# Kernel tuning notes

Hardware: AMD Instinct MI355X
Metric: run time of the kernel (lower is better)

The kernel has to match this reference:

```python
import jax, jax.numpy as jnp
import numpy as np

N = 50000          # nodes per side (variables == clauses here)
IN, HID, OUT = 64, 128, 128
H = 4              # attention heads (self and cross)
P = 2              # num_meta_paths
E = 640000         # edges per graph
NEG = 0.2          # leaky_relu negative slope


def _glorot(key, shape):
    fan = shape[-2] + shape[-1]
    return (jax.random.normal(key, shape) * jnp.sqrt(2.0 / fan)).astype(jnp.float32)


def _ln(x, g, b):
    mu = x.mean(-1, keepdims=True)
    v = ((x - mu) ** 2).mean(-1, keepdims=True)
    return (x - mu) / jnp.sqrt(v + 1e-5) * g + b


def _segment_softmax(s, seg, num):
    # s: [E, H]; softmax over edges sharing the same seg id
    smax = jax.ops.segment_max(s, seg, num_segments=num)
    e = jnp.exp(s - smax[seg])
    den = jax.ops.segment_sum(e, seg, num_segments=num)
    return e / (den[seg] + 1e-16)


def _agg(alpha, feats, src, dst, num):
    # out[d, h, c] = sum_{e: dst[e]=d} alpha[e,h] * feats[src[e], c]
    gathered = feats[src]  # [E, C]
    outs = [jax.ops.segment_sum(alpha[:, h:h + 1] * gathered, dst, num_segments=num)
            for h in range(alpha.shape[1])]
    return jnp.stack(outs, axis=1)  # [num, H, C]


def _hga_self(x, adj, W, att_l, att_r, bias):
    # homogeneous HGAConv with self loops, concat=False (mean over heads)
    n = x.shape[0]
    xl = x @ W.T                      # [N, C]
    al = xl @ att_l                   # [N, H]
    ar = xl @ att_r                   # [N, H]
    loops = jnp.arange(n)
    src = jnp.concatenate([adj[0], loops])
    dst = jnp.concatenate([adj[1], loops])
    score = al[dst] + ar[src]         # edge_score: a_l[adj[1]] + a_r[adj[0]]
    alpha = _segment_softmax(jax.nn.leaky_relu(score, NEG), dst, n)
    out = _agg(alpha, xl, src, dst, n).mean(axis=1)  # [N, C]
    return out + bias


def _hga_cross(xv, xc, adj, Wl, Wr, att_l, att_r, bias):
    # bipartite HGAConv: adj[1] indexes var nodes, adj[0] indexes cls nodes
    n, m = xv.shape[0], xc.shape[0]
    xl = xv @ Wl.T
    xr = xc @ Wr.T
    al = xl @ att_l
    ar = xr @ att_r
    ar_ = xl @ att_r
    al_ = xr @ att_l
    c_idx, v_idx = adj[0], adj[1]
    score = al[v_idx] + ar[c_idx]        # -> normalized per var node
    score_ = ar_[v_idx] + al_[c_idx]     # transposed direction -> per cls node
    alpha = _segment_softmax(jax.nn.leaky_relu(score, NEG), v_idx, n)
    alpha_ = _segment_softmax(jax.nn.leaky_relu(score_, NEG), c_idx, m)
    out_var = _agg(alpha, xr, c_idx, v_idx, n).mean(axis=1) + bias   # [n, OUT]
    out_cls = _agg(alpha_, xl, v_idx, c_idx, m).mean(axis=1) + bias  # [m, OUT]
    return out_var, out_cls


def setup_inputs() -> dict:
    key = jax.random.key(0)
    ks = jax.random.split(key, 32)
    d = {}
    d['x_var'] = jax.random.normal(ks[0], (N, IN), dtype=jnp.float32)
    d['x_cls'] = jax.random.normal(ks[1], (N, IN), dtype=jnp.float32)
    d['mp_var'] = jax.random.randint(ks[2], (P, 2, E), 0, N)
    d['mp_cls'] = jax.random.randint(ks[3], (P, 2, E), 0, N)
    d['adj_pos'] = jax.random.randint(ks[4], (2, E), 0, N)
    d['adj_neg'] = jax.random.randint(ks[5], (2, E), 0, N)
    d['W_var_emb'] = _glorot(ks[6], (HID, IN))
    d['W_cls_emb'] = _glorot(ks[7], (HID, IN))
    d['ln_var_g'] = jnp.ones(HID); d['ln_var_b'] = jnp.zeros(HID)
    d['ln_cls_g'] = jnp.ones(HID); d['ln_cls_b'] = jnp.zeros(HID)
    d['var_pw'] = jnp.ones(P); d['cls_pw'] = jnp.ones(P)
    d['sv_W'] = _glorot(ks[8], (P, HID, HID))
    d['sv_al'] = _glorot(ks[9], (P, HID, H))
    d['sv_ar'] = _glorot(ks[10], (P, HID, H))
    d['sv_b'] = jnp.zeros((P, HID))
    d['sc_W'] = _glorot(ks[11], (P, HID, HID))
    d['sc_al'] = _glorot(ks[12], (P, HID, H))
    d['sc_ar'] = _glorot(ks[13], (P, HID, H))
    d['sc_b'] = jnp.zeros((P, HID))
    d['cp_Wl'] = _glorot(ks[14], (OUT, HID))
    d['cp_Wr'] = _glorot(ks[15], (OUT, HID))
    d['cp_al'] = _glorot(ks[16], (OUT, H))
    d['cp_ar'] = _glorot(ks[17], (OUT, H))
    d['cp_b'] = jnp.zeros(OUT)
    d['cn_Wl'] = _glorot(ks[18], (OUT, HID))
    d['cn_Wr'] = _glorot(ks[19], (OUT, HID))
    d['cn_al'] = _glorot(ks[20], (OUT, H))
    d['cn_ar'] = _glorot(ks[21], (OUT, H))
    d['cn_b'] = jnp.zeros(OUT)
    return d


def reference(x_var, x_cls, mp_var, mp_cls, adj_pos, adj_neg,
              W_var_emb, W_cls_emb, ln_var_g, ln_var_b, ln_cls_g, ln_cls_b,
              var_pw, cls_pw, sv_W, sv_al, sv_ar, sv_b, sc_W, sc_al, sc_ar, sc_b,
              cp_Wl, cp_Wr, cp_al, cp_ar, cp_b, cn_Wl, cn_Wr, cn_al, cn_ar, cn_b):
    xv = x_var @ W_var_emb.T          # [N, HID]
    xc = x_cls @ W_cls_emb.T
    # pre-norm residual self-attention, weighted sum over meta paths
    hv = _ln(xv, ln_var_g, ln_var_b)
    hc = _ln(xc, ln_cls_g, ln_cls_b)
    av = sum(var_pw[p] * _hga_self(hv, mp_var[p], sv_W[p], sv_al[p], sv_ar[p], sv_b[p]) for p in range(P))
    ac = sum(cls_pw[p] * _hga_self(hc, mp_cls[p], sc_W[p], sc_al[p], sc_ar[p], sc_b[p]) for p in range(P))
    xv = xv + av
    xc = xc + ac
    # bipartite cross attention over positive / negative literal edges
    vpos, cpos = _hga_cross(xv, xc, adj_pos, cp_Wl, cp_Wr, cp_al, cp_ar, cp_b)
    vneg, cneg = _hga_cross(xv, xc, adj_neg, cn_Wl, cn_Wr, cn_al, cn_ar, cn_b)
    return jnp.stack([vpos + vneg, cpos + cneg])  # [2, N, OUT]
```

## Files before the change

kernel.cpp:

```cpp
#include <hip/hip_runtime.h>
#include <hip/hip_bf16.h>

#define NN 50000
#define EE 640000
#define NEG 0.2f
#define CAP 64

#define BSH 9
#define NBKT 98
#define FCAP 7168
#define CHUNKA 8192
#define PA_B 79

struct Ptr8 { const int* p[8]; };
struct MArgs { const float* w[8]; const float* al[8]; const float* ar[8]; };

struct SegArg {
    const int* starts;
    const int* counts;
    const unsigned short* srt;
    const float* adst;
    const float* asrc;
    const unsigned short* feats;
    const float* pw;
    int pwi;
    int hasLoop;
};

typedef __attribute__((ext_vector_type(8))) short short8;
typedef __attribute__((ext_vector_type(8))) unsigned short ushort8;
typedef __attribute__((ext_vector_type(4))) float floatx4;

__device__ __forceinline__ unsigned short f2bf(float x) {
    unsigned b = __float_as_uint(x);
    b = b + 0x7fffu + ((b >> 16) & 1u);
    return (unsigned short)(b >> 16);
}

__device__ __forceinline__ float4 leakyexp4(float4 ad, float4 as) {
    float v0 = ad.x + as.x, v1 = ad.y + as.y, v2 = ad.z + as.z, v3 = ad.w + as.w;
    v0 = v0 > 0.f ? v0 : NEG * v0;
    v1 = v1 > 0.f ? v1 : NEG * v1;
    v2 = v2 > 0.f ? v2 : NEG * v2;
    v3 = v3 > 0.f ? v3 : NEG * v3;
    return make_float4(__expf(v0), __expf(v1), __expf(v2), __expf(v3));
}

__global__ void transpose_emb(const float* __restrict__ wev, const float* __restrict__ wec,
                              float* __restrict__ out)
{
    int i = blockIdx.x * 256 + threadIdx.x;
    if (i < 8192) { out[i] = wev[(i & 127) * 64 + (i >> 7)]; return; }
    if (i < 16384) { int j = i - 8192; out[i] = wec[(j & 127) * 64 + (j >> 7)]; }
}

__global__ void make_M(MArgs a, float* __restrict__ Mbuf)
{
    int b = blockIdx.x;
    const float* W  = a.w[b];
    const float* AL = a.al[b];
    const float* AR = a.ar[b];
    for (int e = threadIdx.x; e < 1024; e += 256) {
        int k = e >> 3, h = e & 7;
        const float* att = (h < 4) ? AL : AR;
        int hh = h & 3;
        float s = 0.f;
        for (int c = 0; c < 128; c++) s += W[c * 128 + k] * att[c * 4 + hh];
        Mbuf[b * 1024 + e] = s;
    }
}

__global__ void prep_W(MArgs a, unsigned short* __restrict__ Wbf)
{
    int tid = blockIdx.x * 256 + threadIdx.x;
    int w = tid >> 11;
    int idx = tid & 2047;
    int tile = idx >> 6;
    int lane = idx & 63;
    int ct = tile >> 2, kc = tile & 3;
    int n = ct * 16 + (lane & 15);
    int k0 = kc * 32 + (lane >> 4) * 8;
    const float* src = a.w[w] + n * 128 + k0;
    short8 v;
#pragma unroll
    for (int j = 0; j < 8; j++) v[j] = (short)f2bf(src[j]);
    *(short8*)&Wbf[(size_t)tid * 8] = v;
}

__global__ void embed_ln(const float* __restrict__ x, const float* __restrict__ Wt,
                         const float* __restrict__ g, const float* __restrict__ b,
                         const float* __restrict__ pw, const float* __restrict__ sb,
                         float* __restrict__ F, float* __restrict__ C)
{
    __shared__ float lx[8][64];
    __shared__ float red[2][8][2];
    int c = threadIdx.x;
    int n0 = blockIdx.x * 8;
    for (int t = c; t < 8 * 64; t += 128) {
        lx[t >> 6][t & 63] = x[(size_t)(n0 + (t >> 6)) * 64 + (t & 63)];
    }
    __syncthreads();
    float acc[8];
#pragma unroll
    for (int m = 0; m < 8; m++) acc[m] = 0.f;
    for (int k = 0; k < 64; k++) {
        float w = Wt[k * 128 + c];
#pragma unroll
        for (int m = 0; m < 8; m++) acc[m] += lx[m][k] * w;
    }
    int lane = c & 63, wv = c >> 6;
#pragma unroll
    for (int m = 0; m < 8; m++) {
        float s1 = acc[m], s2 = acc[m] * acc[m];
        for (int off = 32; off; off >>= 1) { s1 += __shfl_xor(s1, off); s2 += __shfl_xor(s2, off); }
        if (lane == 0) { red[wv][m][0] = s1; red[wv][m][1] = s2; }
    }
    __syncthreads();
    float biassum = pw[0] * sb[c] + pw[1] * sb[128 + c];
    float gg = g[c], bb = b[c];
#pragma unroll
    for (int m = 0; m < 8; m++) {
        float s1 = red[0][m][0] + red[1][m][0];
        float s2 = red[0][m][1] + red[1][m][1];
        float mu  = s1 * (1.f / 128.f);
        float var = s2 * (1.f / 128.f) - mu * mu;
        float inv = rsqrtf(var + 1e-5f);
        float v = acc[m];
        size_t idx = (size_t)(n0 + m) * 128 + c;
        F[idx] = v + biassum;
        C[idx] = (v - mu) * inv * gg + bb;
    }
}

__global__ __launch_bounds__(256) void mfma_proj2(
    const float* __restrict__ in,
    const unsigned short* __restrict__ Wp0, const unsigned short* __restrict__ Wp1,
    const float* __restrict__ M0, const float* __restrict__ M1,
    unsigned short* __restrict__ ob0, unsigned short* __restrict__ ob1,
    float4* __restrict__ dl0, float4* __restrict__ dr0,
    float4* __restrict__ dl1, float4* __restrict__ dr1)
{
    __shared__ float ML[2048];

    int t = threadIdx.x;
    for (int i = t; i < 2048; i += 256) ML[i] = (i < 1024) ? M0[i] : M1[i - 1024];
    __syncthreads();

    int w = t >> 6, lane = t & 63;
    int rg = w & 1, chh = w >> 1;
    int ln = lane & 15, quad = lane >> 4;
    int rbase = blockIdx.x * 32 + rg * 16;
    int row = rbase + ln;
    int arow = (row < NN) ? row : (NN - 1);
    const float* MLh = &ML[chh * 1024];

    short8 afrag[4];
    float p[8];
#pragma unroll
    for (int h = 0; h < 8; h++) p[h] = 0.f;
#pragma unroll
    for (int kc = 0; kc < 4; kc++) {
        int k0 = kc * 32 + quad * 8;
        const float* ap = in + (size_t)arow * 128 + k0;
        float av[8];
#pragma unroll
        for (int j = 0; j < 8; j++) av[j] = ap[j];
#pragma unroll
        for (int j = 0; j < 8; j++) {
            afrag[kc][j] = (short)f2bf(av[j]);
            const float* mrow = &MLh[(k0 + j) * 8];
#pragma unroll
            for (int h = 0; h < 8; h++) p[h] += av[j] * mrow[h];
        }
    }
#pragma unroll
    for (int h = 0; h < 8; h++) {
        p[h] += __shfl_xor(p[h], 16);
        p[h] += __shfl_xor(p[h], 32);
    }
    if (quad == 0 && row < NN) {
        if (chh == 0) {
            dl0[row] = make_float4(p[0], p[1], p[2], p[3]);
            dr0[row] = make_float4(p[4], p[5], p[6], p[7]);
        } else {
            dl1[row] = make_float4(p[0], p[1], p[2], p[3]);
            dr1[row] = make_float4(p[4], p[5], p[6], p[7]);
        }
    }

#pragma unroll
    for (int cti = 0; cti < 4; cti++) {
        int ct = chh * 4 + cti;
        floatx4 acc = {0.f, 0.f, 0.f, 0.f};
#pragma unroll
        for (int kc = 0; kc < 4; kc++) {
            short8 bfr = *(const short8*)&Wp0[(size_t)((ct * 4 + kc) * 64 + lane) * 8];
            acc = __builtin_amdgcn_mfma_f32_16x16x32_bf16(afrag[kc], bfr, acc, 0, 0, 0);
        }
#pragma unroll
        for (int r = 0; r < 4; r++) {
            int rr = rbase + quad * 4 + r;
            if (rr < NN) ob0[(size_t)rr * 128 + ct * 16 + ln] = f2bf(acc[r]);
        }
    }
#pragma unroll
    for (int cti = 0; cti < 4; cti++) {
        int ct = chh * 4 + cti;
        floatx4 acc = {0.f, 0.f, 0.f, 0.f};
#pragma unroll
        for (int kc = 0; kc < 4; kc++) {
            short8 bfr = *(const short8*)&Wp1[(size_t)((ct * 4 + kc) * 64 + lane) * 8];
            acc = __builtin_amdgcn_mfma_f32_16x16x32_bf16(afrag[kc], bfr, acc, 0, 0, 0);
        }
#pragma unroll
        for (int r = 0; r < 4; r++) {
            int rr = rbase + quad * 4 + r;
            if (rr < NN) ob1[(size_t)rr * 128 + ct * 16 + ln] = f2bf(acc[r]);
        }
    }
}

__global__ void zero_bcnt(int* __restrict__ p)
{
    int i = blockIdx.x * 256 + threadIdx.x;
    if (i < 8 * NBKT) p[i] = 0;
}

__global__ void bucket_count(Ptr8 dst, int* __restrict__ bcnt)
{
    __shared__ int h[NBKT];
    int l = blockIdx.x / PA_B, cb = blockIdx.x % PA_B;
    const int* dp = dst.p[l];
    for (int i = threadIdx.x; i < NBKT; i += 256) h[i] = 0;
    __syncthreads();
    int e0 = cb * CHUNKA;
    for (int i = threadIdx.x; i < CHUNKA; i += 256) {
        int e = e0 + i;
        if (e < EE) atomicAdd(&h[dp[e] >> BSH], 1);
    }
    __syncthreads();
    for (int i = threadIdx.x; i < NBKT; i += 256)
        if (h[i]) atomicAdd(&bcnt[l * NBKT + i], h[i]);
}

__global__ void bucket_scan(const int* __restrict__ bcnt, int* __restrict__ bstart,
                            int* __restrict__ bcur)
{
    __shared__ int sh[NBKT];
    int l = blockIdx.x;
    for (int i = threadIdx.x; i < NBKT; i += 256) sh[i] = bcnt[l * NBKT + i];
    __syncthreads();
    if (threadIdx.x == 0) {
        int acc = 0;
        for (int i = 0; i < NBKT; i++) { int t = sh[i]; sh[i] = acc; acc += t; }
    }
    __syncthreads();
    for (int i = threadIdx.x; i < NBKT; i += 256) {
        bstart[l * (NBKT + 1) + i] = sh[i];
        bcur[l * NBKT + i] = sh[i];
    }
    if (threadIdx.x == 0) bstart[l * (NBKT + 1) + NBKT] = EE;
}

__global__ void bucket_place(Ptr8 src, Ptr8 dst, int* __restrict__ bcur,
                             unsigned* __restrict__ recs)
{
    __shared__ int h[NBKT];
    __shared__ int base[NBKT];
    int l = blockIdx.x / PA_B, cb = blockIdx.x % PA_B;
    const int* sp = src.p[l];
    const int* dp = dst.p[l];
    for (int i = threadIdx.x; i < NBKT; i += 256) h[i] = 0;
    __syncthreads();
    int e0 = cb * CHUNKA;
    for (int i = threadIdx.x; i < CHUNKA; i += 256) {
        int e = e0 + i;
        if (e < EE) atomicAdd(&h[dp[e] >> BSH], 1);
    }
    __syncthreads();
    for (int i = threadIdx.x; i < NBKT; i += 256) {
        int c = h[i];
        base[i] = c ? atomicAdd(&bcur[l * NBKT + i], c) : 0;
        h[i] = 0;
    }
    __syncthreads();
    unsigned* rl = recs + (size_t)l * EE;
    for (int i = threadIdx.x; i < CHUNKA; i += 256) {
        int e = e0 + i;
        if (e >= EE) continue;
        int d = dp[e];
        int b = d >> BSH;
        int pos = base[b] + atomicAdd(&h[b], 1);
        rl[pos] = ((unsigned)sp[e] << 16) | (unsigned)d;
    }
}

__global__ __launch_bounds__(256) void bucket_final(
    const unsigned* __restrict__ recs, const int* __restrict__ bstart,
    int* __restrict__ starts8, int* __restrict__ counts8,
    unsigned short* __restrict__ sortedU)
{
    __shared__ unsigned R[FCAP];
    __shared__ int cnt[512];
    __shared__ int cur[512];
    __shared__ int psum[256];
    int l = blockIdx.x / NBKT, b = blockIdx.x % NBKT;
    int d0 = b << BSH;
    int nd = min(512, NN - d0);
    int ebase = bstart[l * (NBKT + 1) + b];
    int ecnt  = bstart[l * (NBKT + 1) + b + 1] - ebase;
    const unsigned* rp = recs + (size_t)l * EE + ebase;
    int t = threadIdx.x;
    bool inLds = (ecnt <= FCAP);

    for (int i = t; i < 512; i += 256) cnt[i] = 0;
    __syncthreads();
    for (int i = t; i < ecnt; i += 256) {
        unsigned r = rp[i];
        if (inLds) R[i] = r;
        atomicAdd(&cnt[(r & 0xffffu) - d0], 1);
    }
    __syncthreads();
    int s0 = cnt[2 * t] + cnt[2 * t + 1];
    psum[t] = s0;
    __syncthreads();
    for (int off = 1; off < 256; off <<= 1) {
        int x = (t >= off) ? psum[t - off] : 0;
        __syncthreads();
        psum[t] += x;
        __syncthreads();
    }
    int excl = psum[t] - s0;
    cur[2 * t] = excl;
    cur[2 * t + 1] = excl + cnt[2 * t];
    __syncthreads();
    for (int i = t; i < nd; i += 256) {
        starts8[l * NN + d0 + i] = ebase + cur[i];
        counts8[l * NN + d0 + i] = cnt[i];
    }
    __syncthreads();
    unsigned short* so = sortedU + (size_t)l * EE + ebase;
    for (int i = t; i < ecnt; i += 256) {
        unsigned r = inLds ? R[i] : rp[i];
        int dloc = (int)(r & 0xffffu) - d0;
        int pos = atomicAdd(&cur[dloc], 1);
        so[pos] = (unsigned short)(r >> 16);
    }
}

__global__ __launch_bounds__(256, 6) void agg_fused(
    SegArg A, SegArg B,
    const float* __restrict__ bias0, const float* __restrict__ bias1,
    float* __restrict__ acc, int mode)
{
    __shared__ uint2 pSh[16][CAP];

    int t = threadIdx.x;
    int gid = t >> 4;
    int sub = t & 15;
    int seg = gid & 1;
    int d   = blockIdx.x * 8 + (gid >> 1);

    const int* starts = seg ? B.starts : A.starts;
    const int* counts = seg ? B.counts : A.counts;
    const unsigned short* srt = seg ? B.srt : A.srt;
    const float* adst = seg ? B.adst : A.adst;
    const float* asrc = seg ? B.asrc : A.asrc;
    const unsigned short* feats = seg ? B.feats : A.feats;
    const float* pw = seg ? B.pw : A.pw;
    int pwi = seg ? B.pwi : A.pwi;
    int hasLoop = seg ? B.hasLoop : A.hasLoop;

    int base = starts[d];
    int k = counts[d];
    int kTot = k + hasLoop;

    float4 ad = *(const float4*)(adst + (size_t)d * 4);

    float den0 = 0.f, den1 = 0.f, den2 = 0.f, den3 = 0.f;
    float4 e0 = {0,0,0,0}, e1 = {0,0,0,0}, e2 = {0,0,0,0}, e3 = {0,0,0,0};
    int s0 = 0, s1 = 0, s2 = 0, s3 = 0;
    int ia = sub, ib = sub + 16, ic = sub + 32, id = sub + 48;
    if (ia < kTot) {
        s0 = (ia < k) ? (int)srt[base + ia] : d;
        e0 = leakyexp4(ad, *(const float4*)(asrc + (size_t)s0 * 4));
        den0 += e0.x; den1 += e0.y; den2 += e0.z; den3 += e0.w;
    }
    if (ib < kTot) {
        s1 = (ib < k) ? (int)srt[base + ib] : d;
        e1 = leakyexp4(ad, *(const float4*)(asrc + (size_t)s1 * 4));
        den0 += e1.x; den1 += e1.y; den2 += e1.z; den3 += e1.w;
    }
    if (ic < kTot) {
        s2 = (ic < k) ? (int)srt[base + ic] : d;
        e2 = leakyexp4(ad, *(const float4*)(asrc + (size_t)s2 * 4));
        den0 += e2.x; den1 += e2.y; den2 += e2.z; den3 += e2.w;
    }
    if (id < kTot) {
        s3 = (id < k) ? (int)srt[base + id] : d;
        e3 = leakyexp4(ad, *(const float4*)(asrc + (size_t)s3 * 4));
        den0 += e3.x; den1 += e3.y; den2 += e3.z; den3 += e3.w;
    }
    for (int i = sub + 64; i < kTot; i += 16) {
        int s = (i < k) ? (int)srt[base + i] : d;
        float4 e = leakyexp4(ad, *(const float4*)(asrc + (size_t)s * 4));
        den0 += e.x; den1 += e.y; den2 += e.z; den3 += e.w;
    }
#pragma unroll
    for (int off = 1; off <= 8; off <<= 1) {
        den0 += __shfl_xor(den0, off); den1 += __shfl_xor(den1, off);
        den2 += __shfl_xor(den2, off); den3 += __shfl_xor(den3, off);
    }
    float scale = 0.25f * (pw ? pw[pwi] : 1.0f);
    float r0 = scale / (den0 + 1e-16f);
    float r1 = scale / (den1 + 1e-16f);
    float r2 = scale / (den2 + 1e-16f);
    float r3 = scale / (den3 + 1e-16f);

    if (ia < kTot) pSh[gid][ia] = make_uint2(
        __float_as_uint(e0.x * r0 + e0.y * r1 + e0.z * r2 + e0.w * r3), (unsigned)s0);
    if (ib < kTot) pSh[gid][ib] = make_uint2(
        __float_as_uint(e1.x * r0 + e1.y * r1 + e1.z * r2 + e1.w * r3), (unsigned)s1);
    if (ic < kTot) pSh[gid][ic] = make_uint2(
        __float_as_uint(e2.x * r0 + e2.y * r1 + e2.z * r2 + e2.w * r3), (unsigned)s2);
    if (id < kTot) pSh[gid][id] = make_uint2(
        __float_as_uint(e3.x * r0 + e3.y * r1 + e3.z * r2 + e3.w * r3), (unsigned)s3);

    float a[8];
#pragma unroll
    for (int i = 0; i < 8; i++) a[i] = 0.f;
    const unsigned short* fbase = feats + sub * 8;
    int kW = kTot < CAP ? kTot : CAP;
    int j = 0;
    for (; j + 2 <= kW; j += 2) {
        uint4 pq = *(const uint4*)&pSh[gid][j];
        ushort8 va = *(const ushort8*)(fbase + (size_t)pq.y * 128);
        ushort8 vb = *(const ushort8*)(fbase + (size_t)pq.w * 128);
        float wa = __uint_as_float(pq.x), wb = __uint_as_float(pq.z);
#pragma unroll
        for (int i = 0; i < 8; i++) {
            a[i] += wa * __uint_as_float((unsigned)(unsigned short)va[i] << 16);
            a[i] += wb * __uint_as_float((unsigned)(unsigned short)vb[i] << 16);
        }
    }
    if (j < kW) {
        uint2 ps = pSh[gid][j];
        ushort8 v = *(const ushort8*)(fbase + (size_t)ps.y * 128);
        float wgt = __uint_as_float(ps.x);
#pragma unroll
        for (int i = 0; i < 8; i++)
            a[i] += wgt * __uint_as_float((unsigned)(unsigned short)v[i] << 16);
    }
    for (int jj = CAP; jj < kTot; ++jj) {
        int s = (jj < k) ? (int)srt[base + jj] : d;
        float4 e = leakyexp4(ad, *(const float4*)(asrc + (size_t)s * 4));
        float wgt = e.x * r0 + e.y * r1 + e.z * r2 + e.w * r3;
        ushort8 v = *(const ushort8*)(fbase + (size_t)s * 128);
#pragma unroll
        for (int i = 0; i < 8; i++)
            a[i] += wgt * __uint_as_float((unsigned)(unsigned short)v[i] << 16);
    }

#pragma unroll
    for (int i = 0; i < 8; i++) a[i] += __shfl_xor(a[i], 16);

    if (seg == 0) {
        size_t idx = (size_t)d * 128 + sub * 8;
        float4* ap = (float4*)(acc + idx);
        float4 lo = make_float4(a[0], a[1], a[2], a[3]);
        float4 hi = make_float4(a[4], a[5], a[6], a[7]);
        if (mode) {
            const float4* b0 = (const float4*)(bias0 + sub * 8);
            const float4* b1 = (const float4*)(bias1 + sub * 8);
            float4 c0 = b0[0], c1 = b0[1], d0v = b1[0], d1v = b1[1];
            ap[0] = make_float4(c0.x + d0v.x + lo.x, c0.y + d0v.y + lo.y,
                                c0.z + d0v.z + lo.z, c0.w + d0v.w + lo.w);
            ap[1] = make_float4(c1.x + d1v.x + hi.x, c1.y + d1v.y + hi.y,
                                c1.z + d1v.z + hi.z, c1.w + d1v.w + hi.w);
        } else {
            float4 rr0 = ap[0], rr1 = ap[1];
            ap[0] = make_float4(rr0.x + lo.x, rr0.y + lo.y, rr0.z + lo.z, rr0.w + lo.w);
            ap[1] = make_float4(rr1.x + hi.x, rr1.y + hi.y, rr1.z + hi.z, rr1.w + hi.w);
        }
    }
}

extern "C" void kernel_launch(void* const* d_in, const int* in_sizes, int n_in,
                              void* d_out, int out_size, void* d_ws, size_t ws_size,
                              hipStream_t stream)
{
    const float* x_var   = (const float*)d_in[0];
    const float* x_cls   = (const float*)d_in[1];
    const int*   mp_var  = (const int*)d_in[2];
    const int*   mp_cls  = (const int*)d_in[3];
    const int*   adj_pos = (const int*)d_in[4];
    const int*   adj_neg = (const int*)d_in[5];
    const float* W_var_emb = (const float*)d_in[6];
    const float* W_cls_emb = (const float*)d_in[7];
    const float* ln_var_g = (const float*)d_in[8];
    const float* ln_var_b = (const float*)d_in[9];
    const float* ln_cls_g = (const float*)d_in[10];
    const float* ln_cls_b = (const float*)d_in[11];
    const float* var_pw = (const float*)d_in[12];
    const float* cls_pw = (const float*)d_in[13];
    const float* sv_W  = (const float*)d_in[14];
    const float* sv_al = (const float*)d_in[15];
    const float* sv_ar = (const float*)d_in[16];
    const float* sv_b  = (const float*)d_in[17];
    const float* sc_W  = (const float*)d_in[18];
    const float* sc_al = (const float*)d_in[19];
    const float* sc_ar = (const float*)d_in[20];
    const float* sc_b  = (const float*)d_in[21];
    const float* cp_Wl = (const float*)d_in[22];
    const float* cp_Wr = (const float*)d_in[23];
    const float* cp_al = (const float*)d_in[24];
    const float* cp_ar = (const float*)d_in[25];
    const float* cp_b  = (const float*)d_in[26];
    const float* cn_Wl = (const float*)d_in[27];
    const float* cn_Wr = (const float*)d_in[28];
    const float* cn_al = (const float*)d_in[29];
    const float* cn_ar = (const float*)d_in[30];
    const float* cn_b  = (const float*)d_in[31];

    float* out0 = (float*)d_out;
    float* out1 = out0 + (size_t)NN * 128;

    float* ws = (float*)d_ws;
    size_t off = 0;
    auto alloc = [&](size_t n) { float* p = ws + off; off += n; return p; };
    float* Wt   = alloc(16384);
    float* Mbuf = alloc(8 * 1024);
    unsigned short* Wbf = (unsigned short*)alloc(8 * 8192);
    float* F   = alloc((size_t)NN * 128);
    float* G   = alloc((size_t)NN * 128);
    float* C   = alloc((size_t)NN * 128);
    float* D   = alloc((size_t)NN * 128);
    unsigned short* B1 = (unsigned short*)alloc((size_t)NN * 64);
    unsigned short* B2 = (unsigned short*)alloc((size_t)NN * 64);
    float* dl   = alloc(NN * 4);
    float* dr   = alloc(NN * 4);
    float* dl2  = alloc(NN * 4);
    float* dr2  = alloc(NN * 4);
    float* dl3  = alloc(NN * 4);
    float* dr3  = alloc(NN * 4);
    float* dl4  = alloc(NN * 4);
    float* dr4  = alloc(NN * 4);
    int* counts8 = (int*)alloc(8 * NN);
    int* starts8 = (int*)alloc(8 * NN);
    int* bcnt    = (int*)alloc(8 * NBKT);
    int* bstart  = (int*)alloc(8 * (NBKT + 1));
    int* bcur    = (int*)alloc(8 * NBKT);
    unsigned* recs = (unsigned*)alloc((size_t)8 * EE);
    unsigned short* sortedU = (unsigned short*)alloc((size_t)4 * EE);

    unsigned short* Pc = (unsigned short*)C;
    unsigned short* Pd = (unsigned short*)C + (size_t)NN * 128;

    const float* WtEv = Wt;
    const float* WtEc = Wt + 8192;

    Ptr8 srcP, dstP;
    srcP.p[0] = mp_var;            dstP.p[0] = mp_var + EE;
    srcP.p[1] = mp_var + 2 * EE;   dstP.p[1] = mp_var + 3 * EE;
    srcP.p[2] = mp_cls;            dstP.p[2] = mp_cls + EE;
    srcP.p[3] = mp_cls + 2 * EE;   dstP.p[3] = mp_cls + 3 * EE;
    srcP.p[4] = adj_pos;           dstP.p[4] = adj_pos + EE;
    srcP.p[5] = adj_pos + EE;      dstP.p[5] = adj_pos;
    srcP.p[6] = adj_neg;           dstP.p[6] = adj_neg + EE;
    srcP.p[7] = adj_neg + EE;      dstP.p[7] = adj_neg;

    MArgs ma;
    ma.w[0] = sv_W;           ma.al[0] = sv_al;        ma.ar[0] = sv_ar;
    ma.w[1] = sv_W + 16384;   ma.al[1] = sv_al + 512;  ma.ar[1] = sv_ar + 512;
    ma.w[2] = sc_W;           ma.al[2] = sc_al;        ma.ar[2] = sc_ar;
    ma.w[3] = sc_W + 16384;   ma.al[3] = sc_al + 512;  ma.ar[3] = sc_ar + 512;
    ma.w[4] = cp_Wl;          ma.al[4] = cp_al;        ma.ar[4] = cp_ar;
    ma.w[5] = cp_Wr;          ma.al[5] = cp_al;        ma.ar[5] = cp_ar;
    ma.w[6] = cn_Wl;          ma.al[6] = cn_al;        ma.ar[6] = cn_ar;
    ma.w[7] = cn_Wr;          ma.al[7] = cn_al;        ma.ar[7] = cn_ar;

    zero_bcnt<<<(8 * NBKT + 255) / 256, 256, 0, stream>>>(bcnt);
    bucket_count<<<8 * PA_B, 256, 0, stream>>>(dstP, bcnt);
    bucket_scan<<<8, 256, 0, stream>>>(bcnt, bstart, bcur);
    bucket_place<<<8 * PA_B, 256, 0, stream>>>(srcP, dstP, bcur, recs);
    bucket_final<<<8 * NBKT, 256, 0, stream>>>(recs, bstart, starts8, counts8, sortedU);

    transpose_emb<<<64, 256, 0, stream>>>(W_var_emb, W_cls_emb, Wt);
    make_M<<<8, 256, 0, stream>>>(ma, Mbuf);
    prep_W<<<64, 256, 0, stream>>>(ma, Wbf);
    embed_ln<<<NN / 8, 128, 0, stream>>>(x_var, WtEv, ln_var_g, ln_var_b, var_pw, sv_b, F, C);
    embed_ln<<<NN / 8, 128, 0, stream>>>(x_cls, WtEc, ln_cls_g, ln_cls_b, cls_pw, sc_b, G, D);

    const int PB = (NN + 31) / 32;
    const int AB = NN / 8;

    for (int side = 0; side < 2; ++side) {
        const float* h    = side ? D : C;
        float*       accp = side ? G : F;
        const float* pw   = side ? cls_pw : var_pw;
        int s0 = side * 2, s1 = side * 2 + 1;
        mfma_proj2<<<PB, 256, 0, stream>>>(h, Wbf + s0 * 16384, Wbf + s1 * 16384,
                                           Mbuf + s0 * 1024, Mbuf + s1 * 1024,
                                           B1, B2,
                                           (float4*)dl, (float4*)dr,
                                           (float4*)dl2, (float4*)dr2);
        SegArg SA, SB;
        SA.starts = starts8 + s0 * NN; SA.counts = counts8 + s0 * NN;
        SA.srt = sortedU + (size_t)s0 * EE;
        SA.adst = dl;  SA.asrc = dr;  SA.feats = B1; SA.pw = pw; SA.pwi = 0; SA.hasLoop = 1;
        SB.starts = starts8 + s1 * NN; SB.counts = counts8 + s1 * NN;
        SB.srt = sortedU + (size_t)s1 * EE;
        SB.adst = dl2; SB.asrc = dr2; SB.feats = B2; SB.pw = pw; SB.pwi = 1; SB.hasLoop = 1;
        agg_fused<<<AB, 256, 0, stream>>>(SA, SB, cp_b, cn_b, accp, 0);
    }

    mfma_proj2<<<PB, 256, 0, stream>>>(F, Wbf + 4 * 16384, Wbf + 6 * 16384,
                                       Mbuf + 4 * 1024, Mbuf + 6 * 1024,
                                       B1, Pc,
                                       (float4*)dl, (float4*)dr,
                                       (float4*)dl3, (float4*)dr3);
    mfma_proj2<<<PB, 256, 0, stream>>>(G, Wbf + 5 * 16384, Wbf + 7 * 16384,
                                       Mbuf + 5 * 1024, Mbuf + 7 * 1024,
                                       B2, Pd,
                                       (float4*)dl2, (float4*)dr2,
                                       (float4*)dl4, (float4*)dr4);

    {
        SegArg SA, SB;
        SA.starts = starts8 + 4 * NN; SA.counts = counts8 + 4 * NN;
        SA.srt = sortedU + (size_t)4 * EE;
        SA.adst = dl;  SA.asrc = dr2; SA.feats = B2; SA.pw = nullptr; SA.pwi = 0; SA.hasLoop = 0;
        SB.starts = starts8 + 6 * NN; SB.counts = counts8 + 6 * NN;
        SB.srt = sortedU + (size_t)6 * EE;
        SB.adst = dl3; SB.asrc = dr4; SB.feats = Pd; SB.pw = nullptr; SB.pwi = 0; SB.hasLoop = 0;
        agg_fused<<<AB, 256, 0, stream>>>(SA, SB, cp_b, cn_b, out0, 1);
    }
    {
        SegArg SA, SB;
        SA.starts = starts8 + 5 * NN; SA.counts = counts8 + 5 * NN;
        SA.srt = sortedU + (size_t)5 * EE;
        SA.adst = dl2; SA.asrc = dr;  SA.feats = B1; SA.pw = nullptr; SA.pwi = 0; SA.hasLoop = 0;
        SB.starts = starts8 + 7 * NN; SB.counts = counts8 + 7 * NN;
        SB.srt = sortedU + (size_t)7 * EE;
        SB.adst = dl4; SB.asrc = dr3; SB.feats = Pc; SB.pw = nullptr; SB.pwi = 0; SB.hasLoop = 0;
        agg_fused<<<AB, 256, 0, stream>>>(SA, SB, cp_b, cn_b, out1, 1);
    }
}
```

Baseline: 691.1 us.

## Batch var/cls stages into merged launches and prefetch features in aggregation

Merges the small weight-prep kernels into one launch, runs both embed+LN passes in a single grid, and batches the var and cls self-attention aggregations (and the two cross aggregations) into double-size launches by writing the cls projections to separate buffers. The aggregation kernel now stores weights and source ids in separate shared arrays and issues the first four feature gathers before the softmax denominator is computed, to hide gather latency. It also raises the occupancy hint to 8 blocks per SM and replaces the zeroing kernel with a memset. The cost is higher register pressure from the prefetched fragments and extra buffer usage (Pc/Pd reused earlier).

```diff
diff --git a/kernel.cpp b/kernel.cpp
--- a/kernel.cpp
+++ b/kernel.cpp
@@ -27,6 +27,19 @@
     int hasLoop;
 };
 
+struct ProjArgs {
+    const float* in;
+    const unsigned short* Wp0; const unsigned short* Wp1;
+    const float* M0; const float* M1;
+    unsigned short* ob0; unsigned short* ob1;
+    float4* dl0; float4* dr0; float4* dl1; float4* dr1;
+};
+
+struct EmbArgs {
+    const float* x; const float* Wt; const float* g; const float* b;
+    const float* pw; const float* sb; float* F; float* C;
+};
+
 typedef __attribute__((ext_vector_type(8))) short short8;
 typedef __attribute__((ext_vector_type(8))) unsigned short ushort8;
 typedef __attribute__((ext_vector_type(4))) float floatx4;
@@ -46,65 +59,67 @@
     return make_float4(__expf(v0), __expf(v1), __expf(v2), __expf(v3));
 }
 
-__global__ void transpose_emb(const float* __restrict__ wev, const float* __restrict__ wec,
-                              float* __restrict__ out)
-{
-    int i = blockIdx.x * 256 + threadIdx.x;
-    if (i < 8192) { out[i] = wev[(i & 127) * 64 + (i >> 7)]; return; }
-    if (i < 16384) { int j = i - 8192; out[i] = wec[(j & 127) * 64 + (j >> 7)]; }
-}
-
-__global__ void make_M(MArgs a, float* __restrict__ Mbuf)
+__global__ void prep_all(const float* __restrict__ wev, const float* __restrict__ wec,
+                         float* __restrict__ Wt, MArgs a, float* __restrict__ Mbuf,
+                         unsigned short* __restrict__ Wbf)
 {
     int b = blockIdx.x;
-    const float* W  = a.w[b];
-    const float* AL = a.al[b];
-    const float* AR = a.ar[b];
-    for (int e = threadIdx.x; e < 1024; e += 256) {
-        int k = e >> 3, h = e & 7;
-        const float* att = (h < 4) ? AL : AR;
-        int hh = h & 3;
-        float s = 0.f;
-        for (int c = 0; c < 128; c++) s += W[c * 128 + k] * att[c * 4 + hh];
-        Mbuf[b * 1024 + e] = s;
-    }
-}
-
-__global__ void prep_W(MArgs a, unsigned short* __restrict__ Wbf)
-{
-    int tid = blockIdx.x * 256 + threadIdx.x;
-    int w = tid >> 11;
-    int idx = tid & 2047;
-    int tile = idx >> 6;
-    int lane = idx & 63;
-    int ct = tile >> 2, kc = tile & 3;
-    int n = ct * 16 + (lane & 15);
-    int k0 = kc * 32 + (lane >> 4) * 8;
-    const float* src = a.w[w] + n * 128 + k0;
-    short8 v;
-#pragma unroll
-    for (int j = 0; j < 8; j++) v[j] = (short)f2bf(src[j]);
-    *(short8*)&Wbf[(size_t)tid * 8] = v;
-}
-
-__global__ void embed_ln(const float* __restrict__ x, const float* __restrict__ Wt,
-                         const float* __restrict__ g, const float* __restrict__ b,
-                         const float* __restrict__ pw, const float* __restrict__ sb,
-                         float* __restrict__ F, float* __restrict__ C)
+    if (b < 64) {
+        int i = b * 256 + threadIdx.x;
+        if (i < 8192) { Wt[i] = wev[(i & 127) * 64 + (i >> 7)]; }
+        else { int j = i - 8192; Wt[i] = wec[(j & 127) * 64 + (j >> 7)]; }
+        return;
+    }
+    if (b < 128) {
+        int tid = (b - 64) * 256 + threadIdx.x;
+        int w = tid >> 11;
+        int idx = tid & 2047;
+        int tile = idx >> 6;
+        int lane = idx & 63;
+        int ct = tile >> 2, kc = tile & 3;
+        int n = ct * 16 + (lane & 15);
+        int k0 = kc * 32 + (lane >> 4) * 8;
+        const float* src = a.w[w] + n * 128 + k0;
+        short8 v;
+#pragma unroll
+        for (int j = 0; j < 8; j++) v[j] = (short)f2bf(src[j]);
+        *(short8*)&Wbf[(size_t)tid * 8] = v;
+        return;
+    }
+    {
+        int w = b - 128;
+        const float* W  = a.w[w];
+        const float* AL = a.al[w];
+        const float* AR = a.ar[w];
+        for (int e = threadIdx.x; e < 1024; e += 256) {
+            int k = e >> 3, h = e & 7;
+            const float* att = (h < 4) ? AL : AR;
+            int hh = h & 3;
+            float s = 0.f;
+            for (int c = 0; c < 128; c++) s += W[c * 128 + k] * att[c * 4 + hh];
+            Mbuf[w * 1024 + e] = s;
+        }
+    }
+}
+
+__global__ void embed_ln2(EmbArgs Ea, EmbArgs Eb, int nb)
 {
     __shared__ float lx[8][64];
     __shared__ float red[2][8][2];
+    int half = blockIdx.x >= nb;
+    const EmbArgs E = half ? Eb : Ea;
+    int blk = blockIdx.x - (half ? nb : 0);
     int c = threadIdx.x;
-    int n0 = blockIdx.x * 8;
+    int n0 = blk * 8;
     for (int t = c; t < 8 * 64; t += 128) {
-        lx[t >> 6][t & 63] = x[(size_t)(n0 + (t >> 6)) * 64 + (t & 63)];
+        lx[t >> 6][t & 63] = E.x[(size_t)(n0 + (t >> 6)) * 64 + (t & 63)];
     }
     __syncthreads();
     float acc[8];
 #pragma unroll
     for (int m = 0; m < 8; m++) acc[m] = 0.f;
     for (int k = 0; k < 64; k++) {
-        float w = Wt[k * 128 + c];
+        float w = E.Wt[k * 128 + c];
 #pragma unroll
         for (int m = 0; m < 8; m++) acc[m] += lx[m][k] * w;
     }
@@ -116,8 +131,8 @@
         if (lane == 0) { red[wv][m][0] = s1; red[wv][m][1] = s2; }
     }
     __syncthreads();
-    float biassum = pw[0] * sb[c] + pw[1] * sb[128 + c];
-    float gg = g[c], bb = b[c];
+    float biassum = E.pw[0] * E.sb[c] + E.pw[1] * E.sb[128 + c];
+    float gg = E.g[c], bb = E.b[c];
 #pragma unroll
     for (int m = 0; m < 8; m++) {
         float s1 = red[0][m][0] + red[1][m][0];
@@ -127,29 +142,27 @@
         float inv = rsqrtf(var + 1e-5f);
         float v = acc[m];
         size_t idx = (size_t)(n0 + m) * 128 + c;
-        F[idx] = v + biassum;
-        C[idx] = (v - mu) * inv * gg + bb;
-    }
-}
-
-__global__ __launch_bounds__(256) void mfma_proj2(
-    const float* __restrict__ in,
-    const unsigned short* __restrict__ Wp0, const unsigned short* __restrict__ Wp1,
-    const float* __restrict__ M0, const float* __restrict__ M1,
-    unsigned short* __restrict__ ob0, unsigned short* __restrict__ ob1,
-    float4* __restrict__ dl0, float4* __restrict__ dr0,
-    float4* __restrict__ dl1, float4* __restrict__ dr1)
+        E.F[idx] = v + biassum;
+        E.C[idx] = (v - mu) * inv * gg + bb;
+    }
+}
+
+__global__ __launch_bounds__(256) void mfma_proj2(ProjArgs Pa, ProjArgs Pb, int nb)
 {
     __shared__ float ML[2048];
 
+    int half = blockIdx.x >= nb;
+    const ProjArgs P = half ? Pb : Pa;
+    int blk = blockIdx.x - (half ? nb : 0);
+
     int t = threadIdx.x;
-    for (int i = t; i < 2048; i += 256) ML[i] = (i < 1024) ? M0[i] : M1[i - 1024];
+    for (int i = t; i < 2048; i += 256) ML[i] = (i < 1024) ? P.M0[i] : P.M1[i - 1024];
     __syncthreads();
 
     int w = t >> 6, lane = t & 63;
     int rg = w & 1, chh = w >> 1;
     int ln = lane & 15, quad = lane >> 4;
-    int rbase = blockIdx.x * 32 + rg * 16;
+    int rbase = blk * 32 + rg * 16;
     int row = rbase + ln;
     int arow = (row < NN) ? row : (NN - 1);
     const float* MLh = &ML[chh * 1024];
@@ -161,7 +174,7 @@
 #pragma unroll
     for (int kc = 0; kc < 4; kc++) {
         int k0 = kc * 32 + quad * 8;
-        const float* ap = in + (size_t)arow * 128 + k0;
+        const float* ap = P.in + (size_t)arow * 128 + k0;
         float av[8];
 #pragma unroll
         for (int j = 0; j < 8; j++) av[j] = ap[j];
@@ -180,11 +193,11 @@
     }
     if (quad == 0 && row < NN) {
         if (chh == 0) {
-            dl0[row] = make_float4(p[0], p[1], p[2], p[3]);
-            dr0[row] = make_float4(p[4], p[5], p[6], p[7]);
+            P.dl0[row] = make_float4(p[0], p[1], p[2], p[3]);
+            P.dr0[row] = make_float4(p[4], p[5], p[6], p[7]);
         } else {
-            dl1[row] = make_float4(p[0], p[1], p[2], p[3]);
-            dr1[row] = make_float4(p[4], p[5], p[6], p[7]);
+            P.dl1[row] = make_float4(p[0], p[1], p[2], p[3]);
+            P.dr1[row] = make_float4(p[4], p[5], p[6], p[7]);
         }
     }
 
@@ -194,13 +207,13 @@
         floatx4 acc = {0.f, 0.f, 0.f, 0.f};
 #pragma unroll
         for (int kc = 0; kc < 4; kc++) {
-            short8 bfr = *(const short8*)&Wp0[(size_t)((ct * 4 + kc) * 64 + lane) * 8];
+            short8 bfr = *(const short8*)&P.Wp0[(size_t)((ct * 4 + kc) * 64 + lane) * 8];
             acc = __builtin_amdgcn_mfma_f32_16x16x32_bf16(afrag[kc], bfr, acc, 0, 0, 0);
         }
 #pragma unroll
         for (int r = 0; r < 4; r++) {
             int rr = rbase + quad * 4 + r;
-            if (rr < NN) ob0[(size_t)rr * 128 + ct * 16 + ln] = f2bf(acc[r]);
+            if (rr < NN) P.ob0[(size_t)rr * 128 + ct * 16 + ln] = f2bf(acc[r]);
         }
     }
 #pragma unroll
@@ -209,21 +222,15 @@
         floatx4 acc = {0.f, 0.f, 0.f, 0.f};
 #pragma unroll
         for (int kc = 0; kc < 4; kc++) {
-            short8 bfr = *(const short8*)&Wp1[(size_t)((ct * 4 + kc) * 64 + lane) * 8];
+            short8 bfr = *(const short8*)&P.Wp1[(size_t)((ct * 4 + kc) * 64 + lane) * 8];
             acc = __builtin_amdgcn_mfma_f32_16x16x32_bf16(afrag[kc], bfr, acc, 0, 0, 0);
         }
 #pragma unroll
         for (int r = 0; r < 4; r++) {
             int rr = rbase + quad * 4 + r;
-            if (rr < NN) ob1[(size_t)rr * 128 + ct * 16 + ln] = f2bf(acc[r]);
-        }
-    }
-}
-
-__global__ void zero_bcnt(int* __restrict__ p)
-{
-    int i = blockIdx.x * 256 + threadIdx.x;
-    if (i < 8 * NBKT) p[i] = 0;
+            if (rr < NN) P.ob1[(size_t)rr * 128 + ct * 16 + ln] = f2bf(acc[r]);
+        }
+    }
 }
 
 __global__ void bucket_count(Ptr8 dst, int* __restrict__ bcnt)
@@ -348,62 +355,61 @@
     }
 }
 
-__global__ __launch_bounds__(256, 6) void agg_fused(
-    SegArg A, SegArg B,
+__global__ __launch_bounds__(256, 8) void agg_fused2(
+    SegArg A0, SegArg B0, float* __restrict__ acc0,
+    SegArg A1, SegArg B1, float* __restrict__ acc1,
     const float* __restrict__ bias0, const float* __restrict__ bias1,
-    float* __restrict__ acc, int mode)
-{
-    __shared__ uint2 pSh[16][CAP];
+    int nb, int mode)
+{
+    __shared__ float          wSh[16][CAP + 1];
+    __shared__ unsigned short sSh[16][CAP + 2];
 
     int t = threadIdx.x;
-    int gid = t >> 4;
-    int sub = t & 15;
+    int gid = t >> 4, sub = t & 15;
     int seg = gid & 1;
-    int d   = blockIdx.x * 8 + (gid >> 1);
-
-    const int* starts = seg ? B.starts : A.starts;
-    const int* counts = seg ? B.counts : A.counts;
-    const unsigned short* srt = seg ? B.srt : A.srt;
-    const float* adst = seg ? B.adst : A.adst;
-    const float* asrc = seg ? B.asrc : A.asrc;
-    const unsigned short* feats = seg ? B.feats : A.feats;
-    const float* pw = seg ? B.pw : A.pw;
-    int pwi = seg ? B.pwi : A.pwi;
-    int hasLoop = seg ? B.hasLoop : A.hasLoop;
-
-    int base = starts[d];
-    int k = counts[d];
-    int kTot = k + hasLoop;
-
-    float4 ad = *(const float4*)(adst + (size_t)d * 4);
+    int half = blockIdx.x >= nb;
+    int blk = blockIdx.x - (half ? nb : 0);
+    int d = blk * 8 + (gid >> 1);
+
+    const SegArg S = half ? (seg ? B1 : A1) : (seg ? B0 : A0);
+    float* acc = half ? acc1 : acc0;
+
+    int base = S.starts[d];
+    int k = S.counts[d];
+    int kTot = k + S.hasLoop;
+    int kW = kTot < CAP ? kTot : CAP;
+
+    float4 ad = *(const float4*)(S.adst + (size_t)d * 4);
+
+    int ia = sub, ib = sub + 16, ic = sub + 32, id_ = sub + 48;
+    int s0 = d, s1 = d, s2 = d, s3 = d;
+    if (ia < kTot) { if (ia < k) s0 = (int)S.srt[base + ia]; sSh[gid][ia] = (unsigned short)s0; }
+    if (ib < kTot) { if (ib < k) s1 = (int)S.srt[base + ib]; sSh[gid][ib] = (unsigned short)s1; }
+    if (ic < kTot) { if (ic < k) s2 = (int)S.srt[base + ic]; sSh[gid][ic] = (unsigned short)s2; }
+    if (id_ < kTot){ if (id_ < k) s3 = (int)S.srt[base + id_]; sSh[gid][id_] = (unsigned short)s3; }
+
+    float4 as0 = {0,0,0,0}, as1 = {0,0,0,0}, as2 = {0,0,0,0}, as3 = {0,0,0,0};
+    if (ia < kTot)  as0 = *(const float4*)(S.asrc + (size_t)s0 * 4);
+    if (ib < kTot)  as1 = *(const float4*)(S.asrc + (size_t)s1 * 4);
+    if (ic < kTot)  as2 = *(const float4*)(S.asrc + (size_t)s2 * 4);
+    if (id_ < kTot) as3 = *(const float4*)(S.asrc + (size_t)s3 * 4);
+
+    const unsigned short* fbase = S.feats + sub * 8;
+    ushort8 pf0 = {0,0,0,0,0,0,0,0}, pf1 = pf0, pf2 = pf0, pf3 = pf0;
+    if (0 < kW) { int q = sSh[gid][0]; pf0 = *(const ushort8*)(fbase + (size_t)q * 128); }
+    if (1 < kW) { int q = sSh[gid][1]; pf1 = *(const ushort8*)(fbase + (size_t)q * 128); }
+    if (2 < kW) { int q = sSh[gid][2]; pf2 = *(const ushort8*)(fbase + (size_t)q * 128); }
+    if (3 < kW) { int q = sSh[gid][3]; pf3 = *(const ushort8*)(fbase + (size_t)q * 128); }
 
     float den0 = 0.f, den1 = 0.f, den2 = 0.f, den3 = 0.f;
     float4 e0 = {0,0,0,0}, e1 = {0,0,0,0}, e2 = {0,0,0,0}, e3 = {0,0,0,0};
-    int s0 = 0, s1 = 0, s2 = 0, s3 = 0;
-    int ia = sub, ib = sub + 16, ic = sub + 32, id = sub + 48;
-    if (ia < kTot) {
-        s0 = (ia < k) ? (int)srt[base + ia] : d;
-        e0 = leakyexp4(ad, *(const float4*)(asrc + (size_t)s0 * 4));
-        den0 += e0.x; den1 += e0.y; den2 += e0.z; den3 += e0.w;
-    }
-    if (ib < kTot) {
-        s1 = (ib < k) ? (int)srt[base + ib] : d;
-        e1 = leakyexp4(ad, *(const float4*)(asrc + (size_t)s1 * 4));
-        den0 += e1.x; den1 += e1.y; den2 += e1.z; den3 += e1.w;
-    }
-    if (ic < kTot) {
-        s2 = (ic < k) ? (int)srt[base + ic] : d;
-        e2 = leakyexp4(ad, *(const float4*)(asrc + (size_t)s2 * 4));
-        den0 += e2.x; den1 += e2.y; den2 += e2.z; den3 += e2.w;
-    }
-    if (id < kTot) {
-        s3 = (id < k) ? (int)srt[base + id] : d;
-        e3 = leakyexp4(ad, *(const float4*)(asrc + (size_t)s3 * 4));
-        den0 += e3.x; den1 += e3.y; den2 += e3.z; den3 += e3.w;
-    }
+    if (ia < kTot) { e0 = leakyexp4(ad, as0); den0 += e0.x; den1 += e0.y; den2 += e0.z; den3 += e0.w; }
+    if (ib < kTot) { e1 = leakyexp4(ad, as1); den0 += e1.x; den1 += e1.y; den2 += e1.z; den3 += e1.w; }
+    if (ic < kTot) { e2 = leakyexp4(ad, as2); den0 += e2.x; den1 += e2.y; den2 += e2.z; den3 += e2.w; }
+    if (id_ < kTot){ e3 = leakyexp4(ad, as3); den0 += e3.x; den1 += e3.y; den2 += e3.z; den3 += e3.w; }
     for (int i = sub + 64; i < kTot; i += 16) {
-        int s = (i < k) ? (int)srt[base + i] : d;
-        float4 e = leakyexp4(ad, *(const float4*)(asrc + (size_t)s * 4));
+        int s = (i < k) ? (int)S.srt[base + i] : d;
+        float4 e = leakyexp4(ad, *(const float4*)(S.asrc + (size_t)s * 4));
         den0 += e.x; den1 += e.y; den2 += e.z; den3 += e.w;
     }
 #pragma unroll
@@ -411,49 +417,56 @@
         den0 += __shfl_xor(den0, off); den1 += __shfl_xor(den1, off);
         den2 += __shfl_xor(den2, off); den3 += __shfl_xor(den3, off);
     }
-    float scale = 0.25f * (pw ? pw[pwi] : 1.0f);
+    float scale = 0.25f * (S.pw ? S.pw[S.pwi] : 1.0f);
     float r0 = scale / (den0 + 1e-16f);
     float r1 = scale / (den1 + 1e-16f);
     float r2 = scale / (den2 + 1e-16f);
     float r3 = scale / (den3 + 1e-16f);
 
-    if (ia < kTot) pSh[gid][ia] = make_uint2(
-        __float_as_uint(e0.x * r0 + e0.y * r1 + e0.z * r2 + e0.w * r3), (unsigned)s0);
-    if (ib < kTot) pSh[gid][ib] = make_uint2(
-        __float_as_uint(e1.x * r0 + e1.y * r1 + e1.z * r2 + e1.w * r3), (unsigned)s1);
-    if (ic < kTot) pSh[gid][ic] = make_uint2(
-        __float_as_uint(e2.x * r0 + e2.y * r1 + e2.z * r2 + e2.w * r3), (unsigned)s2);
-    if (id < kTot) pSh[gid][id] = make_uint2(
-        __float_as_uint(e3.x * r0 + e3.y * r1 + e3.z * r2 + e3.w * r3), (unsigned)s3);
+    if (ia < kTot)  wSh[gid][ia]  = e0.x * r0 + e0.y * r1 + e0.z * r2 + e0.w * r3;
+    if (ib < kTot)  wSh[gid][ib]  = e1.x * r0 + e1.y * r1 + e1.z * r2 + e1.w * r3;
+    if (ic < kTot)  wSh[gid][ic]  = e2.x * r0 + e2.y * r1 + e2.z * r2 + e2.w * r3;
+    if (id_ < kTot) wSh[gid][id_] = e3.x * r0 + e3.y * r1 + e3.z * r2 + e3.w * r3;
 
     float a[8];
 #pragma unroll
     for (int i = 0; i < 8; i++) a[i] = 0.f;
-    const unsigned short* fbase = feats + sub * 8;
-    int kW = kTot < CAP ? kTot : CAP;
-    int j = 0;
+    if (0 < kW) { float w = wSh[gid][0];
+#pragma unroll
+        for (int i = 0; i < 8; i++) a[i] += w * __uint_as_float((unsigned)(unsigned short)pf0[i] << 16); }
+    if (1 < kW) { float w = wSh[gid][1];
+#pragma unroll
+        for (int i = 0; i < 8; i++) a[i] += w * __uint_as_float((unsigned)(unsigned short)pf1[i] << 16); }
+    if (2 < kW) { float w = wSh[gid][2];
+#pragma unroll
+        for (int i = 0; i < 8; i++) a[i] += w * __uint_as_float((unsigned)(unsigned short)pf2[i] << 16); }
+    if (3 < kW) { float w = wSh[gid][3];
+#pragma unroll
+        for (int i = 0; i < 8; i++) a[i] += w * __uint_as_float((unsigned)(unsigned short)pf3[i] << 16); }
+
+    int j = 4;
     for (; j + 2 <= kW; j += 2) {
-        uint4 pq = *(const uint4*)&pSh[gid][j];
-        ushort8 va = *(const ushort8*)(fbase + (size_t)pq.y * 128);
-        ushort8 vb = *(const ushort8*)(fbase + (size_t)pq.w * 128);
-        float wa = __uint_as_float(pq.x), wb = __uint_as_float(pq.z);
+        float w0 = wSh[gid][j], w1 = wSh[gid][j + 1];
+        int t0 = sSh[gid][j], t1 = sSh[gid][j + 1];
+        ushort8 va = *(const ushort8*)(fbase + (size_t)t0 * 128);
+        ushort8 vb = *(const ushort8*)(fbase + (size_t)t1 * 128);
 #pragma unroll
         for (int i = 0; i < 8; i++) {
-            a[i] += wa * __uint_as_float((unsigned)(unsigned short)va[i] << 16);
-            a[i] += wb * __uint_as_float((unsigned)(unsigned short)vb[i] << 16);
+            a[i] += w0 * __uint_as_float((unsigned)(unsigned short)va[i] << 16);
+            a[i] += w1 * __uint_as_float((unsigned)(unsigned short)vb[i] << 16);
         }
     }
     if (j < kW) {
-        uint2 ps = pSh[gid][j];
-        ushort8 v = *(const ushort8*)(fbase + (size_t)ps.y * 128);
-        float wgt = __uint_as_float(ps.x);
+        float w0 = wSh[gid][j];
+        int t0 = sSh[gid][j];
+        ushort8 v = *(const ushort8*)(fbase + (size_t)t0 * 128);
 #pragma unroll
         for (int i = 0; i < 8; i++)
-            a[i] += wgt * __uint_as_float((unsigned)(unsigned short)v[i] << 16);
+            a[i] += w0 * __uint_as_float((unsigned)(unsigned short)v[i] << 16);
     }
     for (int jj = CAP; jj < kTot; ++jj) {
-        int s = (jj < k) ? (int)srt[base + jj] : d;
-        float4 e = leakyexp4(ad, *(const float4*)(asrc + (size_t)s * 4));
+        int s = (jj < k) ? (int)S.srt[base + jj] : d;
+        float4 e = leakyexp4(ad, *(const float4*)(S.asrc + (size_t)s * 4));
         float wgt = e.x * r0 + e.y * r1 + e.z * r2 + e.w * r3;
         ushort8 v = *(const ushort8*)(fbase + (size_t)s * 128);
 #pragma unroll
@@ -579,70 +592,65 @@
     ma.w[6] = cn_Wl;          ma.al[6] = cn_al;        ma.ar[6] = cn_ar;
     ma.w[7] = cn_Wr;          ma.al[7] = cn_al;        ma.ar[7] = cn_ar;
 
-    zero_bcnt<<<(8 * NBKT + 255) / 256, 256, 0, stream>>>(bcnt);
+    hipMemsetAsync(bcnt, 0, 8 * NBKT * sizeof(int), stream);
     bucket_count<<<8 * PA_B, 256, 0, stream>>>(dstP, bcnt);
     bucket_scan<<<8, 256, 0, stream>>>(bcnt, bstart, bcur);
     bucket_place<<<8 * PA_B, 256, 0, stream>>>(srcP, dstP, bcur, recs);
     bucket_final<<<8 * NBKT, 256, 0, stream>>>(recs, bstart, starts8, counts8, sortedU);
 
-    transpose_emb<<<64, 256, 0, stream>>>(W_var_emb, W_cls_emb, Wt);
-    make_M<<<8, 256, 0, stream>>>(ma, Mbuf);
-    prep_W<<<64, 256, 0, stream>>>(ma, Wbf);
-    embed_ln<<<NN / 8, 128, 0, stream>>>(x_var, WtEv, ln_var_g, ln_var_b, var_pw, sv_b, F, C);
-    embed_ln<<<NN / 8, 128, 0, stream>>>(x_cls, WtEc, ln_cls_g, ln_cls_b, cls_pw, sc_b, G, D);
+    prep_all<<<136, 256, 0, stream>>>(W_var_emb, W_cls_emb, Wt, ma, Mbuf, Wbf);
+
+    EmbArgs Ev = { x_var, WtEv, ln_var_g, ln_var_b, var_pw, sv_b, F, C };
+    EmbArgs Ec = { x_cls, WtEc, ln_cls_g, ln_cls_b, cls_pw, sc_b, G, D };
+    embed_ln2<<<2 * (NN / 8), 128, 0, stream>>>(Ev, Ec, NN / 8);
 
     const int PB = (NN + 31) / 32;
     const int AB = NN / 8;
 
-    for (int side = 0; side < 2; ++side) {
-        const float* h    = side ? D : C;
-        float*       accp = side ? G : F;
-        const float* pw   = side ? cls_pw : var_pw;
-        int s0 = side * 2, s1 = side * 2 + 1;
-        mfma_proj2<<<PB, 256, 0, stream>>>(h, Wbf + s0 * 16384, Wbf + s1 * 16384,
-                                           Mbuf + s0 * 1024, Mbuf + s1 * 1024,
-                                           B1, B2,
-                                           (float4*)dl, (float4*)dr,
-                                           (float4*)dl2, (float4*)dr2);
-        SegArg SA, SB;
-        SA.starts = starts8 + s0 * NN; SA.counts = counts8 + s0 * NN;
-        SA.srt = sortedU + (size_t)s0 * EE;
-        SA.adst = dl;  SA.asrc = dr;  SA.feats = B1; SA.pw = pw; SA.pwi = 0; SA.hasLoop = 1;
-        SB.starts = starts8 + s1 * NN; SB.counts = counts8 + s1 * NN;
-        SB.srt = sortedU + (size_t)s1 * EE;
-        SB.adst = dl2; SB.asrc = dr2; SB.feats = B2; SB.pw = pw; SB.pwi = 1; SB.hasLoop = 1;
-        agg_fused<<<AB, 256, 0, stream>>>(SA, SB, cp_b, cn_b, accp, 0);
-    }
-
-    mfma_proj2<<<PB, 256, 0, stream>>>(F, Wbf + 4 * 16384, Wbf + 6 * 16384,
-                                       Mbuf + 4 * 1024, Mbuf + 6 * 1024,
-                                       B1, Pc,
-                                       (float4*)dl, (float4*)dr,
-                                       (float4*)dl3, (float4*)dr3);
-    mfma_proj2<<<PB, 256, 0, stream>>>(G, Wbf + 5 * 16384, Wbf + 7 * 16384,
-                                       Mbuf + 5 * 1024, Mbuf + 7 * 1024,
-                                       B2, Pd,
-                                       (float4*)dl2, (float4*)dr2,
-                                       (float4*)dl4, (float4*)dr4);
+    ProjArgs Ps0 = { C, Wbf + 0 * 16384, Wbf + 1 * 16384, Mbuf + 0 * 1024, Mbuf + 1 * 1024,
+                     B1, B2, (float4*)dl, (float4*)dr, (float4*)dl2, (float4*)dr2 };
+    mfma_proj2<<<PB, 256, 0, stream>>>(Ps0, Ps0, PB);
+    ProjArgs Ps1 = { D, Wbf + 2 * 16384, Wbf + 3 * 16384, Mbuf + 2 * 1024, Mbuf + 3 * 1024,
+                     Pc, Pd, (float4*)dl3, (float4*)dr3, (float4*)dl4, (float4*)dr4 };
+    mfma_proj2<<<PB, 256, 0, stream>>>(Ps1, Ps1, PB);
 
     {
-        SegArg SA, SB;
-        SA.starts = starts8 + 4 * NN; SA.counts = counts8 + 4 * NN;
-        SA.srt = sortedU + (size_t)4 * EE;
-        SA.adst = dl;  SA.asrc = dr2; SA.feats = B2; SA.pw = nullptr; SA.pwi = 0; SA.hasLoop = 0;
-        SB.starts = starts8 + 6 * NN; SB.counts = counts8 + 6 * NN;
-        SB.srt = sortedU + (size_t)6 * EE;
-        SB.adst = dl3; SB.asrc = dr4; SB.feats = Pd; SB.pw = nullptr; SB.pwi = 0; SB.hasLoop = 0;
-        agg_fused<<<AB, 256, 0, stream>>>(SA, SB, cp_b, cn_b, out0, 1);
-    }
+        SegArg VA, VB, CA, CB;
+        VA.starts = starts8 + 0 * NN; VA.counts = counts8 + 0 * NN;
+        VA.srt = sortedU + (size_t)0 * EE;
+        VA.adst = dl;  VA.asrc = dr;  VA.feats = B1; VA.pw = var_pw; VA.pwi = 0; VA.hasLoop = 1;
+        VB.starts = starts8 + 1 * NN; VB.counts = counts8 + 1 * NN;
+        VB.srt = sortedU + (size_t)1 * EE;
+        VB.adst = dl2; VB.asrc = dr2; VB.feats = B2; VB.pw = var_pw; VB.pwi = 1; VB.hasLoop = 1;
+        CA.starts = starts8 + 2 * NN; CA.counts = counts8 + 2 * NN;
+        CA.srt = sortedU + (size_t)2 * EE;
+        CA.adst = dl3; CA.asrc = dr3; CA.feats = Pc; CA.pw = cls_pw; CA.pwi = 0; CA.hasLoop = 1;
+        CB.starts = starts8 + 3 * NN; CB.counts = counts8 + 3 * NN;
+        CB.srt = sortedU + (size_t)3 * EE;
+        CB.adst = dl4; CB.asrc = dr4; CB.feats = Pd; CB.pw = cls_pw; CB.pwi = 1; CB.hasLoop = 1;
+        agg_fused2<<<2 * AB, 256, 0, stream>>>(VA, VB, F, CA, CB, G, cp_b, cn_b, AB, 0);
+    }
+
+    ProjArgs Pc0 = { F, Wbf + 4 * 16384, Wbf + 6 * 16384, Mbuf + 4 * 1024, Mbuf + 6 * 1024,
+                     B1, Pc, (float4*)dl, (float4*)dr, (float4*)dl3, (float4*)dr3 };
+    ProjArgs Pc1 = { G, Wbf + 5 * 16384, Wbf + 7 * 16384, Mbuf + 5 * 1024, Mbuf + 7 * 1024,
+                     B2, Pd, (float4*)dl2, (float4*)dr2, (float4*)dl4, (float4*)dr4 };
+    mfma_proj2<<<2 * PB, 256, 0, stream>>>(Pc0, Pc1, PB);
+
     {
-        SegArg SA, SB;
-        SA.starts = starts8 + 5 * NN; SA.counts = counts8 + 5 * NN;
-        SA.srt = sortedU + (size_t)5 * EE;
-        SA.adst = dl2; SA.asrc = dr;  SA.feats = B1; SA.pw = nullptr; SA.pwi = 0; SA.hasLoop = 0;
-        SB.starts = starts8 + 7 * NN; SB.counts = counts8 + 7 * NN;
-        SB.srt = sortedU + (size_t)7 * EE;
-        SB.adst = dl4; SB.asrc = dr3; SB.feats = Pc; SB.pw = nullptr; SB.pwi = 0; SB.hasLoop = 0;
-        agg_fused<<<AB, 256, 0, stream>>>(SA, SB, cp_b, cn_b, out1, 1);
-    }
-}
+        SegArg OA, OB, PA, PBs;
+        OA.starts = starts8 + 4 * NN; OA.counts = counts8 + 4 * NN;
+        OA.srt = sortedU + (size_t)4 * EE;
+        OA.adst = dl;  OA.asrc = dr2; OA.feats = B2; OA.pw = nullptr; OA.pwi = 0; OA.hasLoop = 0;
+        OB.starts = starts8 + 6 * NN; OB.counts = counts8 + 6 * NN;
+        OB.srt = sortedU + (size_t)6 * EE;
+        OB.adst = dl3; OB.asrc = dr4; OB.feats = Pd; OB.pw = nullptr; OB.pwi = 0; OB.hasLoop = 0;
+        PA.starts = starts8 + 5 * NN; PA.counts = counts8 + 5 * NN;
+        PA.srt = sortedU + (size_t)5 * EE;
+        PA.adst = dl2; PA.asrc = dr;  PA.feats = B1; PA.pw = nullptr; PA.pwi = 0; PA.hasLoop = 0;
+        PBs.starts = starts8 + 7 * NN; PBs.counts = counts8 + 7 * NN;
+        PBs.srt = sortedU + (size_t)7 * EE;
+        PBs.adst = dl4; PBs.asrc = dr3; PBs.feats = Pc; PBs.pw = nullptr; PBs.pwi = 0; PBs.hasLoop = 0;
+        agg_fused2<<<2 * AB, 256, 0, stream>>>(OA, OB, out0, PA, PBs, out1, cp_b, cn_b, AB, 1);
+    }
+}
```

Result: slower. 887.5 us (+28.4%).
